# Optimization experiments

Hardware: AMD Instinct MI355X
Metric: run time of the kernel (lower is better)

Reference implementation:

```python
import jax, jax.numpy as jnp
import numpy as np
from jax import lax

N = 14
K = 512
NUM_CLASSES = 10
TAO = 0.5 / (N * N)
BETA = 2.0


def make_t_p(n=N, tao=TAO, beta=BETA):
    # t_p[i, j, a, b] = tao * max(1 - beta * (|a-i| + |b-j|) / n, -1)
    idx = jnp.arange(n, dtype=jnp.float32)
    d = (jnp.abs(idx[:, None, None, None] - idx[None, None, :, None])
         + jnp.abs(idx[None, :, None, None] - idx[None, None, None, :]))
    return (tao * jnp.maximum(1.0 - beta * d / n, -1.0)).astype(jnp.float32)


def masked_output(x, t_p):
    # Vectorized equivalent of computeMaskedOutput: global spatial argmax per
    # (batch, channel) selects a template, then masked = relu(x * template).
    B, H, W, C = x.shape
    flat_idx = jnp.argmax(x.reshape(B, H * W, C), axis=1)      # [B, C]
    pi, pj = flat_idx // W, flat_idx % W
    tpl = t_p[pi, pj]                                          # [B, C, H, W]
    tpl = jnp.transpose(tpl, (0, 2, 3, 1))                     # [B, H, W, C]
    masked = jax.nn.relu(x * tpl)
    return masked, x, tpl


def compute_loss(x, pos_templates, act_sums, cls_sums, gt):
    # Fused segment-sum form of the original nested python loops.
    classes = jnp.zeros(NUM_CLASSES, x.dtype).at[gt].add(1.0)  # bincount
    cls_new = cls_sums + classes
    means = jnp.mean(x, axis=(1, 2))                           # [B, C]
    onehot = jax.nn.one_hot(gt, NUM_CLASSES, dtype=x.dtype)    # [B, 10]
    act_new = act_sums + means.T @ onehot                      # [C, 10]
    # divide_no_nan
    fm = jnp.where(cls_new[None, :] == 0, 0.0,
                   act_new / jnp.where(cls_new[None, :] == 0, 1.0, cls_new[None, :]))
    fclass = jnp.argmax(fm, axis=1)                            # [C]
    match = fclass[None, :] == gt[:, None]                     # [B, C]
    pt = jax.nn.relu(pos_templates)
    # relu(t_n) == 0 since t_n is strictly negative
    loss = jnp.where(match[:, None, None, :], pt, 0.0)
    return loss, act_new, cls_new


def forward(inputs, gt, conv_w, conv_b, dense_w, dense_b,
            activation_sums_1, activation_sums_2, class_sums_1, class_sums_2):
    t_p = make_t_p()
    raw_map = inputs  # base_model treated as identity on its feature map
    x1, X1_relu, pos_t1 = masked_output(raw_map, t_p)
    x3 = jax.nn.relu(lax.conv_general_dilated(
        x1, conv_w, window_strides=(1, 1), padding='SAME',
        dimension_numbers=('NHWC', 'HWIO', 'NHWC')) + conv_b)
    x2, X2_relu, pos_t2 = masked_output(x3, t_p)
    pooled = lax.reduce_window(x2, -jnp.inf, lax.max,
                               (1, 2, 2, 1), (1, 2, 2, 1), 'VALID')
    flat = pooled.reshape(pooled.shape[0], -1)
    probs = jax.nn.softmax(flat @ dense_w + dense_b, axis=-1)
    loss1, as1, cs1 = compute_loss(x1, pos_t1, activation_sums_1, class_sums_1, gt)
    loss2, as2, cs2 = compute_loss(x2, pos_t2, activation_sums_2, class_sums_2, gt)
    return probs, x1, x2, loss1, loss2, raw_map, pos_t1


def setup_inputs() -> dict:
    key = jax.random.key(0)
    ks = jax.random.split(key, 4)
    B = 128
    inputs = jax.random.uniform(ks[0], (B, N, N, K), dtype=jnp.float32)
    gt = jax.random.randint(ks[1], (B,), 0, NUM_CLASSES)
    conv_w = jax.random.normal(ks[2], (3, 3, K, K), dtype=jnp.float32) * 0.02
    conv_b = jnp.zeros((K,), jnp.float32)
    D = (N // 2) * (N // 2) * K  # 25088
    dense_w = jax.random.normal(ks[3], (D, NUM_CLASSES), dtype=jnp.float32) * 0.02
    dense_b = jnp.zeros((NUM_CLASSES,), jnp.float32)
    return {
        'inputs': inputs, 'gt': gt,
        'conv_w': conv_w, 'conv_b': conv_b,
        'dense_w': dense_w, 'dense_b': dense_b,
        'activation_sums_1': jnp.zeros((K, NUM_CLASSES), jnp.float32),
        'activation_sums_2': jnp.zeros((K, NUM_CLASSES), jnp.float32),
        'class_sums_1': jnp.zeros((NUM_CLASSES,), jnp.float32),
        'class_sums_2': jnp.zeros((NUM_CLASSES,), jnp.float32),
    }


def reference(inputs, gt, conv_w, conv_b, dense_w, dense_b,
              activation_sums_1, activation_sums_2, class_sums_1, class_sums_2):
    return forward(inputs, gt, conv_w, conv_b, dense_w, dense_b,
                   activation_sums_1, activation_sums_2,
                   class_sums_1, class_sums_2)
```

## Files before the change

kernel.cpp:

```cpp
#include <hip/hip_runtime.h>
#include <hip/hip_bf16.h>
#include <stdint.h>

#define TAO_F (0.5f/196.0f)

typedef short s16x8 __attribute__((ext_vector_type(8)));
typedef float f32x4 __attribute__((ext_vector_type(4)));
typedef __attribute__((address_space(1))) const unsigned int u32_g;
typedef __attribute__((address_space(3))) unsigned int u32_l;

__device__ __forceinline__ void async_ld16(const void* g, void* l) {
  __builtin_amdgcn_global_load_lds((u32_g*)g, (u32_l*)l, 16, 0, 0);
}

__device__ __forceinline__ void fuse1_body(
    int bid, const float* __restrict__ in, const int* __restrict__ gt,
    float* __restrict__ o_raw, float* __restrict__ o_x1, float* __restrict__ o_t1,
    __hip_bfloat16* __restrict__ x1p, float* __restrict__ act1,
    int* __restrict__ idx1, uint8_t* smem) {
  int b = bid >> 4, cg = bid & 15;
  int t = threadIdx.x;
  int c4 = t & 7, sp = t >> 3;
  int c0 = cg * 32 + c4 * 4;
  int cq = c0 >> 2;
  float (*rv)[8][4] = (float(*)[8][4])smem;
  int   (*ri)[8][4] = (int(*)[8][4])(smem + 4096);

  const float4* ip = (const float4*)in + (size_t)b * 196 * 128;
  float4* rp = (float4*)o_raw + (size_t)b * 196 * 128;

  float bv[4] = {-1e30f, -1e30f, -1e30f, -1e30f};
  int bix[4] = {0, 0, 0, 0};
  for (int s = sp; s < 196; s += 32) {
    float4 v = ip[s * 128 + cq];
    rp[s * 128 + cq] = v;
    float vv[4] = {v.x, v.y, v.z, v.w};
#pragma unroll
    for (int k = 0; k < 4; ++k)
      if (vv[k] > bv[k]) { bv[k] = vv[k]; bix[k] = s; }
  }
#pragma unroll
  for (int k = 0; k < 4; ++k) { rv[sp][c4][k] = bv[k]; ri[sp][c4][k] = bix[k]; }
  __syncthreads();
  for (int st = 16; st >= 1; st >>= 1) {
    if (sp < st) {
#pragma unroll
      for (int k = 0; k < 4; ++k) {
        float v1 = rv[sp][c4][k], v2 = rv[sp + st][c4][k];
        int i1 = ri[sp][c4][k], i2 = ri[sp + st][c4][k];
        if (v2 > v1 || (v2 == v1 && i2 < i1)) { rv[sp][c4][k] = v2; ri[sp][c4][k] = i2; }
      }
    }
    __syncthreads();
  }
  int pi[4], pj[4];
#pragma unroll
  for (int k = 0; k < 4; ++k) {
    int id = ri[0][c4][k];
    pi[k] = id / 14; pj[k] = id - pi[k] * 14;
  }
  if (sp == 0)
    *(int4*)&idx1[b * 512 + c0] = make_int4(ri[0][c4][0], ri[0][c4][1], ri[0][c4][2], ri[0][c4][3]);
  __syncthreads();

  float4* xo = (float4*)o_x1 + (size_t)b * 196 * 128;
  float4* to = (float4*)o_t1 + (size_t)b * 196 * 128;
  float sm[4] = {0.f, 0.f, 0.f, 0.f};
  for (int s = sp; s < 196; s += 32) {
    int i = s / 14, j = s - i * 14;
    float4 x = ip[s * 128 + cq];
    float xx[4] = {x.x, x.y, x.z, x.w};
    float tp[4], mm[4];
#pragma unroll
    for (int k = 0; k < 4; ++k) {
      int di = i - pi[k]; di = di < 0 ? -di : di;
      int dj = j - pj[k]; dj = dj < 0 ? -dj : dj;
      tp[k] = TAO_F * fmaxf(1.0f - (float)(di + dj) * (1.0f / 7.0f), -1.0f);
      mm[k] = fmaxf(xx[k] * tp[k], 0.0f);
      sm[k] += mm[k];
    }
    xo[s * 128 + cq] = make_float4(mm[0], mm[1], mm[2], mm[3]);
    to[s * 128 + cq] = make_float4(tp[0], tp[1], tp[2], tp[3]);
    union { ushort4 u4; __hip_bfloat16 h[4]; } cv;
#pragma unroll
    for (int k = 0; k < 4; ++k) cv.h[k] = __float2bfloat16(mm[k]);
    *(ushort4*)&x1p[((size_t)(b * 16 + i + 1) * 16 + (j + 1)) * 512 + c0] = cv.u4;
  }
#pragma unroll
  for (int k = 0; k < 4; ++k) rv[sp][c4][k] = sm[k];
  __syncthreads();
  for (int st = 16; st >= 1; st >>= 1) {
    if (sp < st) {
#pragma unroll
      for (int k = 0; k < 4; ++k) rv[sp][c4][k] += rv[sp + st][c4][k];
    }
    __syncthreads();
  }
  if (sp == 0) {
    int g = gt[b];
#pragma unroll
    for (int k = 0; k < 4; ++k)
      atomicAdd(&act1[(c0 + k) * 10 + g], rv[0][c4][k] * (1.0f / 196.0f));
  }
}

__global__ __launch_bounds__(256) void k_pre(
    const float* __restrict__ w, __hip_bfloat16* __restrict__ wT,
    const float* __restrict__ in, const int* __restrict__ gt,
    float* __restrict__ o_raw, float* __restrict__ o_x1, float* __restrict__ o_t1,
    __hip_bfloat16* __restrict__ x1p, float* __restrict__ act1, int* __restrict__ idx1) {
  __shared__ uint8_t smem[16640];
  if (blockIdx.x < 576) {
    float (*tile)[65] = (float(*)[65])smem;
    int bid = blockIdx.x;
    int r = bid / 64; int rem = bid - r * 64;
    int cib = (rem >> 3) * 64, cob = (rem & 7) * 64;
    int tid = threadIdx.x;
    int col = tid & 63, rw = tid >> 6;
#pragma unroll
    for (int p = 0; p < 16; ++p) {
      int row = p * 4 + rw;
      tile[row][col] = w[(size_t)(r * 512 + cib + row) * 512 + cob + col];
    }
    __syncthreads();
#pragma unroll
    for (int p = 0; p < 16; ++p) {
      int row = p * 4 + rw;
      wT[(size_t)(r * 512 + cob + row) * 512 + cib + col] = __float2bfloat16(tile[col][row]);
    }
  } else {
    fuse1_body(blockIdx.x - 576, in, gt, o_raw, o_x1, o_t1, x1p, act1, idx1, smem);
  }
}

__global__ __launch_bounds__(256, 3) void k_gemm(const __hip_bfloat16* __restrict__ x1p,
                                                 const __hip_bfloat16* __restrict__ wT,
                                                 const float* __restrict__ conv_b,
                                                 float* __restrict__ x3) {
  int bid = blockIdx.x;
  int nt4 = bid & 3; int mt196 = bid >> 2;
  int m0 = mt196 * 128, co0 = nt4 * 128;
  int tid = threadIdx.x;
  int lane = tid & 63;

  __shared__ short As[128 * 64];
  __shared__ short Bs[128 * 64];

  int srow = tid >> 3;
  int sslot = tid & 7;
  int sx = ((sslot ^ (srow & 7)) * 8);

  int baseA[4];
#pragma unroll
  for (int p = 0; p < 4; ++p) {
    int m = m0 + p * 32 + srow;
    int b = m / 196; int s = m - b * 196; int i = s / 14; int j = s - i * 14;
    baseA[p] = ((b * 16 + i + 1) * 16 + (j + 1)) * 512;
  }
  int baseB[4];
#pragma unroll
  for (int p = 0; p < 4; ++p) baseB[p] = (co0 + p * 32 + srow) * 512;

  f32x4 acc[4][4] = {};

  int m_off = (tid >> 7) * 64;
  int n_off = ((tid >> 6) & 1) * 64;
  int q = lane >> 4;
  int l16 = lane & 15;

  for (int r = 0; r < 9; ++r) {
    int offr = ((r / 3) * 16 + (r % 3) - 17) * 512;
    int wbase = r * 512 * 512;
    for (int cb = 0; cb < 8; ++cb) {
      int ko = cb * 64;
      __syncthreads();
#pragma unroll
      for (int p = 0; p < 4; ++p) {
        async_ld16(x1p + (baseA[p] + offr + ko + sx),
                   &As[(p * 32 + srow) * 64 + sslot * 8]);
        async_ld16(wT + (wbase + baseB[p] + ko + sx),
                   &Bs[(p * 32 + srow) * 64 + sslot * 8]);
      }
      __syncthreads();
#pragma unroll
      for (int kk = 0; kk < 2; ++kk) {
        s16x8 af[4], bf[4];
#pragma unroll
        for (int tt = 0; tt < 4; ++tt) {
          int rowa = m_off + tt * 16 + l16;
          int sa = (kk * 4 + q) ^ (rowa & 7);
          af[tt] = *(const s16x8*)&As[rowa * 64 + sa * 8];
          int rowb = n_off + tt * 16 + l16;
          int sb = (kk * 4 + q) ^ (rowb & 7);
          bf[tt] = *(const s16x8*)&Bs[rowb * 64 + sb * 8];
        }
#pragma unroll
        for (int mt = 0; mt < 4; ++mt)
#pragma unroll
          for (int nt = 0; nt < 4; ++nt)
            acc[mt][nt] = __builtin_amdgcn_mfma_f32_16x16x32_bf16(af[mt], bf[nt], acc[mt][nt], 0, 0, 0);
      }
    }
  }
#pragma unroll
  for (int nt = 0; nt < 4; ++nt) {
    int col = co0 + n_off + nt * 16 + l16;
    float bias = conv_b[col];
#pragma unroll
    for (int mt = 0; mt < 4; ++mt) {
      int mrow = m0 + m_off + mt * 16 + q * 4;
#pragma unroll
      for (int rg = 0; rg < 4; ++rg) {
        float v = acc[mt][nt][rg] + bias;
        x3[(size_t)(mrow + rg) * 512 + col] = fmaxf(v, 0.0f);
      }
    }
  }
}

__global__ __launch_bounds__(256) void k_fuse2(
    const float* __restrict__ x3, const int* __restrict__ gt,
    const float* __restrict__ dw, float* __restrict__ o_x2,
    float* __restrict__ act2, float* __restrict__ logits, int* __restrict__ idx2) {
  __shared__ float4 vals[196][8];
  __shared__ float rv[32][8][4];
  __shared__ int   ri[32][8][4];
  __shared__ float red[10];
  int bid = blockIdx.x; int b = bid >> 4, cg = bid & 15;
  int t = threadIdx.x, c4 = t & 7, sp = t >> 3;
  int c0 = cg * 32 + c4 * 4, cq = c0 >> 2;
  const float4* ip = (const float4*)x3 + (size_t)b * 196 * 128;

  float bv[4] = {-1e30f, -1e30f, -1e30f, -1e30f};
  int bix[4] = {0, 0, 0, 0};
  for (int s = sp; s < 196; s += 32) {
    float4 v = ip[s * 128 + cq];
    vals[s][c4] = v;
    float vv[4] = {v.x, v.y, v.z, v.w};
#pragma unroll
    for (int k = 0; k < 4; ++k)
      if (vv[k] > bv[k]) { bv[k] = vv[k]; bix[k] = s; }
  }
#pragma unroll
  for (int k = 0; k < 4; ++k) { rv[sp][c4][k] = bv[k]; ri[sp][c4][k] = bix[k]; }
  __syncthreads();
  for (int st = 16; st >= 1; st >>= 1) {
    if (sp < st) {
#pragma unroll
      for (int k = 0; k < 4; ++k) {
        float v1 = rv[sp][c4][k], v2 = rv[sp + st][c4][k];
        int i1 = ri[sp][c4][k], i2 = ri[sp + st][c4][k];
        if (v2 > v1 || (v2 == v1 && i2 < i1)) { rv[sp][c4][k] = v2; ri[sp][c4][k] = i2; }
      }
    }
    __syncthreads();
  }
  int pi[4], pj[4];
#pragma unroll
  for (int k = 0; k < 4; ++k) {
    int id = ri[0][c4][k];
    pi[k] = id / 14; pj[k] = id - pi[k] * 14;
  }
  if (sp == 0)
    *(int4*)&idx2[b * 512 + c0] = make_int4(ri[0][c4][0], ri[0][c4][1], ri[0][c4][2], ri[0][c4][3]);
  if (t < 10) red[t] = 0.f;
  __syncthreads();

  float4* xo = (float4*)o_x2 + (size_t)b * 196 * 128;
  float sm[4] = {0.f, 0.f, 0.f, 0.f};
  for (int s = sp; s < 196; s += 32) {
    int i = s / 14, j = s - i * 14;
    float4 x = vals[s][c4];
    float xx[4] = {x.x, x.y, x.z, x.w};
    float mm[4];
#pragma unroll
    for (int k = 0; k < 4; ++k) {
      int di = i - pi[k]; di = di < 0 ? -di : di;
      int dj = j - pj[k]; dj = dj < 0 ? -dj : dj;
      float tp = TAO_F * fmaxf(1.0f - (float)(di + dj) * (1.0f / 7.0f), -1.0f);
      mm[k] = fmaxf(xx[k] * tp, 0.0f);
      sm[k] += mm[k];
    }
    float4 m4 = make_float4(mm[0], mm[1], mm[2], mm[3]);
    xo[s * 128 + cq] = m4;
    vals[s][c4] = m4;
  }
#pragma unroll
  for (int k = 0; k < 4; ++k) rv[sp][c4][k] = sm[k];
  __syncthreads();
  for (int st = 16; st >= 1; st >>= 1) {
    if (sp < st) {
#pragma unroll
      for (int k = 0; k < 4; ++k) rv[sp][c4][k] += rv[sp + st][c4][k];
    }
    __syncthreads();
  }
  if (sp == 0) {
    int g = gt[b];
#pragma unroll
    for (int k = 0; k < 4; ++k)
      atomicAdd(&act2[(c0 + k) * 10 + g], rv[0][c4][k] * (1.0f / 196.0f));
  }

  float a[10] = {0.f,0.f,0.f,0.f,0.f,0.f,0.f,0.f,0.f,0.f};
  for (int pp = sp; pp < 49; pp += 32) {
    int ii = pp / 7, jj = pp - ii * 7;
    int s00 = (2 * ii) * 14 + 2 * jj;
    float4 v00 = vals[s00][c4], v01 = vals[s00 + 1][c4];
    float4 v10 = vals[s00 + 14][c4], v11 = vals[s00 + 15][c4];
    float pmx = fmaxf(fmaxf(v00.x, v01.x), fmaxf(v10.x, v11.x));
    float pmy = fmaxf(fmaxf(v00.y, v01.y), fmaxf(v10.y, v11.y));
    float pmz = fmaxf(fmaxf(v00.z, v01.z), fmaxf(v10.z, v11.z));
    float pmw = fmaxf(fmaxf(v00.w, v01.w), fmaxf(v10.w, v11.w));
    const float* wr = dw + ((size_t)((ii * 7 + jj) * 512 + c0)) * 10;
#pragma unroll
    for (int t2 = 0; t2 < 10; ++t2)
      a[t2] += pmx * wr[t2] + pmy * wr[10 + t2] + pmz * wr[20 + t2] + pmw * wr[30 + t2];
  }
  int lane = t & 63;
#pragma unroll
  for (int t2 = 0; t2 < 10; ++t2) {
    float v = a[t2];
    for (int off = 32; off > 0; off >>= 1) v += __shfl_down(v, off);
    if (lane == 0) atomicAdd(&red[t2], v);
  }
  __syncthreads();
  if (t < 10) atomicAdd(&logits[b * 10 + t], red[t]);
}

__global__ void k_stats(const float* __restrict__ act1, const float* __restrict__ act2,
                        const float* __restrict__ as1, const float* __restrict__ as2,
                        const float* __restrict__ cs1, const float* __restrict__ cs2,
                        const int* __restrict__ gt, const float* __restrict__ logits,
                        const float* __restrict__ db, int* __restrict__ fc1,
                        int* __restrict__ fc2, float* __restrict__ o_probs) {
  __shared__ int scnt[10];
  int tid = threadIdx.x;
  if (tid < 10) scnt[tid] = 0;
  __syncthreads();
  if (tid < 128) atomicAdd(&scnt[gt[tid]], 1);
  __syncthreads();
  int c = tid;
  float best1 = -1e30f, best2 = -1e30f; int b1 = 0, b2 = 0;
#pragma unroll
  for (int g = 0; g < 10; ++g) {
    float cnt = (float)scnt[g];
    float cn1 = cs1[g] + cnt;
    float cn2 = cs2[g] + cnt;
    float a1 = act1[c * 10 + g] + as1[c * 10 + g];
    float a2 = act2[c * 10 + g] + as2[c * 10 + g];
    float f1 = (cn1 == 0.f) ? 0.f : a1 / cn1;
    float f2 = (cn2 == 0.f) ? 0.f : a2 / cn2;
    if (f1 > best1) { best1 = f1; b1 = g; }
    if (f2 > best2) { best2 = f2; b2 = g; }
  }
  fc1[c] = b1; fc2[c] = b2;
  if (tid < 128) {
    float l[10]; float m = -1e30f;
#pragma unroll
    for (int t2 = 0; t2 < 10; ++t2) { l[t2] = logits[tid * 10 + t2] + db[t2]; m = fmaxf(m, l[t2]); }
    float s = 0.f;
#pragma unroll
    for (int t2 = 0; t2 < 10; ++t2) { l[t2] = expf(l[t2] - m); s += l[t2]; }
    float inv = 1.0f / s;
#pragma unroll
    for (int t2 = 0; t2 < 10; ++t2) o_probs[tid * 10 + t2] = l[t2] * inv;
  }
}

__global__ __launch_bounds__(256) void k_loss(
    const int* __restrict__ idx1, const int* __restrict__ idx2,
    const int* __restrict__ fc1, const int* __restrict__ fc2,
    const int* __restrict__ gt, float* __restrict__ o1, float* __restrict__ o2) {
  int bid = blockIdx.x;
  int b = bid / 14, i = bid - b * 14;
  int t = threadIdx.x;
  int cgp = t & 127, jh = t >> 7;
  int c0 = cgp * 4;
  int g = gt[b];
  int4 i1 = *(const int4*)&idx1[b * 512 + c0];
  int4 i2 = *(const int4*)&idx2[b * 512 + c0];
  int4 f1 = *(const int4*)&fc1[c0];
  int4 f2 = *(const int4*)&fc2[c0];
  float ms1[4] = {f1.x == g ? 1.f : 0.f, f1.y == g ? 1.f : 0.f,
                  f1.z == g ? 1.f : 0.f, f1.w == g ? 1.f : 0.f};
  float ms2[4] = {f2.x == g ? 1.f : 0.f, f2.y == g ? 1.f : 0.f,
                  f2.z == g ? 1.f : 0.f, f2.w == g ? 1.f : 0.f};
  int p1i[4], p1j[4], p2i[4], p2j[4];
  int ia1[4] = {i1.x, i1.y, i1.z, i1.w};
  int ia2[4] = {i2.x, i2.y, i2.z, i2.w};
#pragma unroll
  for (int k = 0; k < 4; ++k) {
    p1i[k] = ia1[k] / 14; p1j[k] = ia1[k] - p1i[k] * 14;
    p2i[k] = ia2[k] / 14; p2j[k] = ia2[k] - p2i[k] * 14;
  }
  float4* w1 = (float4*)o1 + ((size_t)b * 196 + i * 14) * 128 + (c0 >> 2);
  float4* w2 = (float4*)o2 + ((size_t)b * 196 + i * 14) * 128 + (c0 >> 2);
  for (int jj = 0; jj < 7; ++jj) {
    int j = jh * 7 + jj;
    float r1[4], r2[4];
#pragma unroll
    for (int k = 0; k < 4; ++k) {
      int d1i = i - p1i[k]; d1i = d1i < 0 ? -d1i : d1i;
      int d1j = j - p1j[k]; d1j = d1j < 0 ? -d1j : d1j;
      int d2i = i - p2i[k]; d2i = d2i < 0 ? -d2i : d2i;
      int d2j = j - p2j[k]; d2j = d2j < 0 ? -d2j : d2j;
      r1[k] = ms1[k] * (TAO_F * fmaxf(1.0f - (float)(d1i + d1j) * (1.0f / 7.0f), 0.0f));
      r2[k] = ms2[k] * (TAO_F * fmaxf(1.0f - (float)(d2i + d2j) * (1.0f / 7.0f), 0.0f));
    }
    w1[(size_t)j * 128] = make_float4(r1[0], r1[1], r1[2], r1[3]);
    w2[(size_t)j * 128] = make_float4(r2[0], r2[1], r2[2], r2[3]);
  }
}

extern "C" void kernel_launch(void* const* d_in, const int* in_sizes, int n_in,
                              void* d_out, int out_size, void* d_ws, size_t ws_size,
                              hipStream_t stream) {
  const float* inputs  = (const float*)d_in[0];
  const int*   gt      = (const int*)d_in[1];
  const float* conv_w  = (const float*)d_in[2];
  const float* conv_b  = (const float*)d_in[3];
  const float* dense_w = (const float*)d_in[4];
  const float* dense_b = (const float*)d_in[5];
  const float* as1     = (const float*)d_in[6];
  const float* as2     = (const float*)d_in[7];
  const float* cs1     = (const float*)d_in[8];
  const float* cs2     = (const float*)d_in[9];

  float* out = (float*)d_out;
  const size_t S = 12845056;
  float* o_probs = out;
  float* o_x1  = out + 1280;
  float* o_x2  = o_x1 + S;
  float* o_l1  = o_x2 + S;
  float* o_l2  = o_l1 + S;
  float* o_raw = o_l2 + S;
  float* o_t1  = o_raw + S;

  uint8_t* w8 = (uint8_t*)d_ws;
  __hip_bfloat16* x1p = (__hip_bfloat16*)w8;
  float* x3  = (float*)(w8 + 33554432);
  __hip_bfloat16* wT = (__hip_bfloat16*)(w8 + 84934656);
  int*   idx1 = (int*)(w8 + 89653248);
  int*   idx2 = (int*)(w8 + 89915392);
  float* act1 = (float*)(w8 + 90177536);
  float* act2 = (float*)(w8 + 90198016);
  float* logits = (float*)(w8 + 90218496);
  int*   fc1  = (int*)(w8 + 90223616);
  int*   fc2  = (int*)(w8 + 90225664);

  hipMemsetAsync(x1p, 0, 33554432, stream);
  hipMemsetAsync(act1, 0, 46080, stream);

  k_pre   <<<576 + 2048, 256, 0, stream>>>(conv_w, wT, inputs, gt, o_raw, o_x1, o_t1,
                                           x1p, act1, idx1);
  k_gemm  <<<784, 256, 0, stream>>>(x1p, wT, conv_b, x3);
  k_fuse2 <<<2048, 256, 0, stream>>>(x3, gt, dense_w, o_x2, act2, logits, idx2);
  k_stats <<<1, 512, 0, stream>>>(act1, act2, as1, as2, cs1, cs2, gt, logits, dense_b,
                                  fc1, fc2, o_probs);
  k_loss  <<<1792, 256, 0, stream>>>(idx1, idx2, fc1, fc2, gt, o_l1, o_l2);
}
```

Measured before the change: 594.5 us.

## Switch conv implicit GEMM from bf16 to scaled fp8 MFMA

Activations and transposed weights are quantized to fp8 with fixed power-of-two prescales, and the conv GEMM now uses the 16x16x128 f8f6f4 scaled MFMA with K-blocks of 128. The result is rescaled in the epilogue. This halves GEMM operand bytes and doubles MFMA throughput per instruction, and also shrinks the padded buffer memset. The cost is reduced precision in the conv output, which may exceed tolerance and affect downstream argmax/class decisions.

```diff
diff --git a/kernel.cpp b/kernel.cpp
--- a/kernel.cpp
+++ b/kernel.cpp
@@ -3,20 +3,30 @@
 #include <stdint.h>
 
 #define TAO_F (0.5f/196.0f)
-
-typedef short s16x8 __attribute__((ext_vector_type(8)));
+#define A_SC 512.0f
+#define B_SC 64.0f
+#define EPI (1.0f/32768.0f)
+
 typedef float f32x4 __attribute__((ext_vector_type(4)));
+typedef int   i32x4 __attribute__((ext_vector_type(4)));
+typedef int   i32x8 __attribute__((ext_vector_type(8)));
 typedef __attribute__((address_space(1))) const unsigned int u32_g;
 typedef __attribute__((address_space(3))) unsigned int u32_l;
 
 __device__ __forceinline__ void async_ld16(const void* g, void* l) {
   __builtin_amdgcn_global_load_lds((u32_g*)g, (u32_l*)l, 16, 0, 0);
+}
+
+__device__ __forceinline__ unsigned int pk_fp8x4(float a, float b, float c, float d) {
+  int r = __builtin_amdgcn_cvt_pk_fp8_f32(a, b, 0, false);
+  r = __builtin_amdgcn_cvt_pk_fp8_f32(c, d, r, true);
+  return (unsigned int)r;
 }
 
 __device__ __forceinline__ void fuse1_body(
     int bid, const float* __restrict__ in, const int* __restrict__ gt,
     float* __restrict__ o_raw, float* __restrict__ o_x1, float* __restrict__ o_t1,
-    __hip_bfloat16* __restrict__ x1p, float* __restrict__ act1,
+    uint8_t* __restrict__ x1p8, float* __restrict__ act1,
     int* __restrict__ idx1, uint8_t* smem) {
   int b = bid >> 4, cg = bid & 15;
   int t = threadIdx.x;
@@ -81,10 +91,8 @@
     }
     xo[s * 128 + cq] = make_float4(mm[0], mm[1], mm[2], mm[3]);
     to[s * 128 + cq] = make_float4(tp[0], tp[1], tp[2], tp[3]);
-    union { ushort4 u4; __hip_bfloat16 h[4]; } cv;
-#pragma unroll
-    for (int k = 0; k < 4; ++k) cv.h[k] = __float2bfloat16(mm[k]);
-    *(ushort4*)&x1p[((size_t)(b * 16 + i + 1) * 16 + (j + 1)) * 512 + c0] = cv.u4;
+    *(unsigned int*)&x1p8[((size_t)(b * 16 + i + 1) * 16 + (j + 1)) * 512 + c0] =
+        pk_fp8x4(mm[0] * A_SC, mm[1] * A_SC, mm[2] * A_SC, mm[3] * A_SC);
   }
 #pragma unroll
   for (int k = 0; k < 4; ++k) rv[sp][c4][k] = sm[k];
@@ -105,10 +113,10 @@
 }
 
 __global__ __launch_bounds__(256) void k_pre(
-    const float* __restrict__ w, __hip_bfloat16* __restrict__ wT,
+    const float* __restrict__ w, uint8_t* __restrict__ wT8,
     const float* __restrict__ in, const int* __restrict__ gt,
     float* __restrict__ o_raw, float* __restrict__ o_x1, float* __restrict__ o_t1,
-    __hip_bfloat16* __restrict__ x1p, float* __restrict__ act1, int* __restrict__ idx1) {
+    uint8_t* __restrict__ x1p8, float* __restrict__ act1, int* __restrict__ idx1) {
   __shared__ uint8_t smem[16640];
   if (blockIdx.x < 576) {
     float (*tile)[65] = (float(*)[65])smem;
@@ -123,18 +131,21 @@
       tile[row][col] = w[(size_t)(r * 512 + cib + row) * 512 + cob + col];
     }
     __syncthreads();
-#pragma unroll
-    for (int p = 0; p < 16; ++p) {
-      int row = p * 4 + rw;
-      wT[(size_t)(r * 512 + cob + row) * 512 + cib + col] = __float2bfloat16(tile[col][row]);
+    int cw = tid & 15, rw2 = tid >> 4;
+#pragma unroll
+    for (int p = 0; p < 4; ++p) {
+      int co = p * 16 + rw2;
+      unsigned int pk = pk_fp8x4(tile[cw * 4 + 0][co] * B_SC, tile[cw * 4 + 1][co] * B_SC,
+                                 tile[cw * 4 + 2][co] * B_SC, tile[cw * 4 + 3][co] * B_SC);
+      *(unsigned int*)&wT8[(size_t)(r * 512 + cob + co) * 512 + cib + cw * 4] = pk;
     }
   } else {
-    fuse1_body(blockIdx.x - 576, in, gt, o_raw, o_x1, o_t1, x1p, act1, idx1, smem);
-  }
-}
-
-__global__ __launch_bounds__(256, 3) void k_gemm(const __hip_bfloat16* __restrict__ x1p,
-                                                 const __hip_bfloat16* __restrict__ wT,
+    fuse1_body(blockIdx.x - 576, in, gt, o_raw, o_x1, o_t1, x1p8, act1, idx1, smem);
+  }
+}
+
+__global__ __launch_bounds__(256, 3) void k_gemm(const uint8_t* __restrict__ x1p8,
+                                                 const uint8_t* __restrict__ wT8,
                                                  const float* __restrict__ conv_b,
                                                  float* __restrict__ x3) {
   int bid = blockIdx.x;
@@ -143,12 +154,12 @@
   int tid = threadIdx.x;
   int lane = tid & 63;
 
-  __shared__ short As[128 * 64];
-  __shared__ short Bs[128 * 64];
+  __shared__ uint8_t As[128 * 128];
+  __shared__ uint8_t Bs[128 * 128];
 
   int srow = tid >> 3;
   int sslot = tid & 7;
-  int sx = ((sslot ^ (srow & 7)) * 8);
+  int sx = (sslot ^ (srow & 7)) * 16;
 
   int baseA[4];
 #pragma unroll
@@ -171,35 +182,38 @@
   for (int r = 0; r < 9; ++r) {
     int offr = ((r / 3) * 16 + (r % 3) - 17) * 512;
     int wbase = r * 512 * 512;
-    for (int cb = 0; cb < 8; ++cb) {
-      int ko = cb * 64;
+    for (int cb = 0; cb < 4; ++cb) {
+      int ko = cb * 128;
       __syncthreads();
 #pragma unroll
       for (int p = 0; p < 4; ++p) {
-        async_ld16(x1p + (baseA[p] + offr + ko + sx),
-                   &As[(p * 32 + srow) * 64 + sslot * 8]);
-        async_ld16(wT + (wbase + baseB[p] + ko + sx),
-                   &Bs[(p * 32 + srow) * 64 + sslot * 8]);
+        async_ld16(x1p8 + (baseA[p] + offr + ko + sx),
+                   &As[(p * 32 + srow) * 128 + sslot * 16]);
+        async_ld16(wT8 + (wbase + baseB[p] + ko + sx),
+                   &Bs[(p * 32 + srow) * 128 + sslot * 16]);
       }
       __syncthreads();
-#pragma unroll
-      for (int kk = 0; kk < 2; ++kk) {
-        s16x8 af[4], bf[4];
-#pragma unroll
-        for (int tt = 0; tt < 4; ++tt) {
-          int rowa = m_off + tt * 16 + l16;
-          int sa = (kk * 4 + q) ^ (rowa & 7);
-          af[tt] = *(const s16x8*)&As[rowa * 64 + sa * 8];
-          int rowb = n_off + tt * 16 + l16;
-          int sb = (kk * 4 + q) ^ (rowb & 7);
-          bf[tt] = *(const s16x8*)&Bs[rowb * 64 + sb * 8];
-        }
-#pragma unroll
-        for (int mt = 0; mt < 4; ++mt)
-#pragma unroll
-          for (int nt = 0; nt < 4; ++nt)
-            acc[mt][nt] = __builtin_amdgcn_mfma_f32_16x16x32_bf16(af[mt], bf[nt], acc[mt][nt], 0, 0, 0);
+      i32x8 af[4], bf[4];
+#pragma unroll
+      for (int tt = 0; tt < 4; ++tt) {
+        int rowa = m_off + tt * 16 + l16;
+        int e = rowa & 7;
+        i32x4 lo = *(const i32x4*)&As[rowa * 128 + ((2 * q) ^ e) * 16];
+        i32x4 hi = *(const i32x4*)&As[rowa * 128 + ((2 * q + 1) ^ e) * 16];
+        af[tt] = (i32x8){lo.x, lo.y, lo.z, lo.w, hi.x, hi.y, hi.z, hi.w};
+        int rowb = n_off + tt * 16 + l16;
+        int eb = rowb & 7;
+        i32x4 blo = *(const i32x4*)&Bs[rowb * 128 + ((2 * q) ^ eb) * 16];
+        i32x4 bhi = *(const i32x4*)&Bs[rowb * 128 + ((2 * q + 1) ^ eb) * 16];
+        bf[tt] = (i32x8){blo.x, blo.y, blo.z, blo.w, bhi.x, bhi.y, bhi.z, bhi.w};
       }
+#pragma unroll
+      for (int mt = 0; mt < 4; ++mt)
+#pragma unroll
+        for (int nt = 0; nt < 4; ++nt)
+          acc[mt][nt] = __builtin_amdgcn_mfma_scale_f32_16x16x128_f8f6f4(
+              af[mt], bf[nt], acc[mt][nt], 0, 0,
+              0, 0x7F7F7F7F, 0, 0x7F7F7F7F);
     }
   }
 #pragma unroll
@@ -211,7 +225,7 @@
       int mrow = m0 + m_off + mt * 16 + q * 4;
 #pragma unroll
       for (int rg = 0; rg < 4; ++rg) {
-        float v = acc[mt][nt][rg] + bias;
+        float v = acc[mt][nt][rg] * EPI + bias;
         x3[(size_t)(mrow + rg) * 512 + col] = fmaxf(v, 0.0f);
       }
     }
@@ -438,23 +452,23 @@
   float* o_t1  = o_raw + S;
 
   uint8_t* w8 = (uint8_t*)d_ws;
-  __hip_bfloat16* x1p = (__hip_bfloat16*)w8;
-  float* x3  = (float*)(w8 + 33554432);
-  __hip_bfloat16* wT = (__hip_bfloat16*)(w8 + 84934656);
-  int*   idx1 = (int*)(w8 + 89653248);
-  int*   idx2 = (int*)(w8 + 89915392);
-  float* act1 = (float*)(w8 + 90177536);
-  float* act2 = (float*)(w8 + 90198016);
-  float* logits = (float*)(w8 + 90218496);
-  int*   fc1  = (int*)(w8 + 90223616);
-  int*   fc2  = (int*)(w8 + 90225664);
-
-  hipMemsetAsync(x1p, 0, 33554432, stream);
+  uint8_t* x1p8 = w8;
+  float*   x3   = (float*)(w8 + 16777216);
+  uint8_t* wT8  = w8 + 68157440;
+  int*   idx1 = (int*)(w8 + 70516736);
+  int*   idx2 = (int*)(w8 + 70778880);
+  float* act1 = (float*)(w8 + 71041024);
+  float* act2 = (float*)(w8 + 71061504);
+  float* logits = (float*)(w8 + 71081984);
+  int*   fc1  = (int*)(w8 + 71087104);
+  int*   fc2  = (int*)(w8 + 71089152);
+
+  hipMemsetAsync(x1p8, 0, 16777216, stream);
   hipMemsetAsync(act1, 0, 46080, stream);
 
-  k_pre   <<<576 + 2048, 256, 0, stream>>>(conv_w, wT, inputs, gt, o_raw, o_x1, o_t1,
-                                           x1p, act1, idx1);
-  k_gemm  <<<784, 256, 0, stream>>>(x1p, wT, conv_b, x3);
+  k_pre   <<<576 + 2048, 256, 0, stream>>>(conv_w, wT8, inputs, gt, o_raw, o_x1, o_t1,
+                                           x1p8, act1, idx1);
+  k_gemm  <<<784, 256, 0, stream>>>(x1p8, wT8, conv_b, x3);
   k_fuse2 <<<2048, 256, 0, stream>>>(x3, gt, dense_w, o_x2, act2, logits, idx2);
   k_stats <<<1, 512, 0, stream>>>(act1, act2, as1, as2, cs1, cs2, gt, logits, dense_b,
                                   fc1, fc2, o_probs);
```

Result: faster. 546.6 us (-8.1%).
